# Kernel optimization log

Hardware: AMD Instinct MI355X
Metric: run time of the kernel (lower is better)

Reference implementation:

```python
import jax, jax.numpy as jnp
import numpy as np

HIDDEN = 256
BATCH = 8
N_A = 2048
N_B = 2048


def setup_inputs() -> dict:
    key = jax.random.key(0)
    ks = jax.random.split(key, 9)
    s = 1.0 / np.sqrt(HIDDEN)  # torch Linear default init scale
    return {
        "A": jax.random.normal(ks[0], (BATCH, N_A, HIDDEN), dtype=jnp.float32),
        "B": jax.random.normal(ks[1], (BATCH, N_B, HIDDEN), dtype=jnp.float32),
        "mask_B": jax.random.randint(ks[2], (BATCH, N_B), 0, 2, dtype=jnp.int32),
        "Wq": jax.random.uniform(ks[3], (HIDDEN, HIDDEN), jnp.float32, -s, s),
        "bq": jax.random.uniform(ks[4], (HIDDEN,), jnp.float32, -s, s),
        "Wk": jax.random.uniform(ks[5], (HIDDEN, HIDDEN), jnp.float32, -s, s),
        "bk": jax.random.uniform(ks[6], (HIDDEN,), jnp.float32, -s, s),
        "Wv": jax.random.uniform(ks[7], (HIDDEN, HIDDEN), jnp.float32, -s, s),
        "bv": jax.random.uniform(ks[8], (HIDDEN,), jnp.float32, -s, s),
    }


def reference(A, B, mask_B, Wq, bq, Wk, bk, Wv, bv):
    # QKV projections (torch Linear: x @ W.T + b)
    Q = A @ Wq.T + bq          # [B, N_A, H]
    K = B @ Wk.T + bk          # [B, N_B, H]
    V = B @ Wv.T + bv          # [B, N_B, H]
    scale = 1.0 / jnp.sqrt(jnp.asarray(Q.shape[-1], Q.dtype))
    scores = jnp.einsum("bnh,bmh->bnm", Q, K) * scale  # [B, N_A, N_B]
    neg_inf = jnp.finfo(scores.dtype).min
    scores = jnp.where(mask_B[:, None, :] == 0, neg_inf, scores)
    attn = jax.nn.softmax(scores, axis=-1)
    out = jnp.einsum("bnm,bmh->bnh", attn, V)          # [B, N_A, H]
    return out
```

## Files before the change

### kernel.cpp

```cpp
#include <hip/hip_runtime.h>


typedef __attribute__((ext_vector_type(8))) __bf16 bf16x8;
typedef __attribute__((ext_vector_type(4))) __bf16 bf16x4;
typedef __attribute__((ext_vector_type(4))) float f32x4;

#if __has_builtin(__builtin_amdgcn_exp2f)
#define EXP2(x) __builtin_amdgcn_exp2f(x)
#else
#define EXP2(x) exp2f(x)
#endif

#define MFMA16(a, b, c) __builtin_amdgcn_mfma_f32_16x16x32_bf16((a), (b), (c), 0, 0, 0)

typedef const __attribute__((address_space(1))) char gas_char;
typedef __attribute__((address_space(3))) char las_char;

static __device__ __forceinline__ void gload16(const void* g, void* l) {
  __builtin_amdgcn_global_load_lds((gas_char*)g, (las_char*)l, 16, 0, 0);
}

static __device__ __forceinline__ bf16x8 pack8(f32x4 a, f32x4 b) {
  bf16x8 r;
  r[0] = (__bf16)a[0]; r[1] = (__bf16)a[1]; r[2] = (__bf16)a[2]; r[3] = (__bf16)a[3];
  r[4] = (__bf16)b[0]; r[5] = (__bf16)b[1]; r[6] = (__bf16)b[2]; r[7] = (__bf16)b[3];
  return r;
}

__global__ __launch_bounds__(256) void wprep_kernel(
    const float* __restrict__ Wq, const float* __restrict__ Wk,
    const float* __restrict__ Wv, const int* __restrict__ mask,
    __bf16* __restrict__ Wb, float* __restrict__ mb) {
  const int bid = blockIdx.x;
  if (bid < 96) {
    int c = bid * 256 + threadIdx.x;
    int w_id = c >> 13;
    int j = c & 8191;
    const float* __restrict__ W = (w_id == 0) ? Wq : (w_id == 1 ? Wk : Wv);
    int n = j >> 5;
    int c5 = j & 31;
    int qtr = c5 >> 3;
    int k8 = (c5 & 7) << 3;
    const float* wp = &W[n * 256 + qtr * 64 + k8];
    f32x4 w0 = *(const f32x4*)wp;
    f32x4 w1 = *(const f32x4*)(wp + 4);
    if (w_id == 0) {
      const float cs = 0.090168440f;
      w0[0] *= cs; w0[1] *= cs; w0[2] *= cs; w0[3] *= cs;
      w1[0] *= cs; w1[1] *= cs; w1[2] *= cs; w1[3] *= cs;
    }
    int kx = k8 ^ ((n & 7) << 3);
    *(bf16x8*)&Wb[(size_t)w_id * 65536 + qtr * 16384 + n * 64 + kx] =
        pack8(w0, w1);
  } else {
    int i = (bid - 96) * 256 + threadIdx.x;
    if (i < 8 * 2048) mb[i] = (mask[i] != 0) ? 0.0f : -1.0e30f;
  }
}

__global__ __launch_bounds__(256, 2) void proj_kernel(
    const float* __restrict__ A, const float* __restrict__ Bm,
    const __bf16* __restrict__ Wb,
    const float* __restrict__ bq, const float* __restrict__ bk,
    const float* __restrict__ bv,
    __bf16* __restrict__ QF, __bf16* __restrict__ KF, __bf16* __restrict__ VF) {
  extern __shared__ char smem[];
  const int pid = blockIdx.x;
  const bool isQ = (pid < 256);
  const int rb = (pid & 255) << 6;
  const float* __restrict__ X = isQ ? A : Bm;
  const int tid = threadIdx.x;
  const int w = tid >> 6, l = tid & 63, lo = l & 15, g = l >> 4;
  const int r0 = rb + w * 16;

  bf16x8 xf[8];
#pragma unroll
  for (int q8 = 0; q8 < 8; ++q8) {
    const float* xp = &X[(r0 + lo) * 256 + q8 * 32 + g * 8];
    xf[q8] = pack8(*(const f32x4*)xp, *(const f32x4*)(xp + 4));
  }

  #define STAGEW(srcbase, buf)                                                \
    {                                                                         \
      const char* gw = (srcbase) + w * 1024 + l * 16;                         \
      char* lw = smem + (buf)*32768 + w * 1024;                               \
      gload16(gw, lw);                                                        \
      gload16(gw + 4096, lw + 4096);                                          \
      gload16(gw + 8192, lw + 8192);                                          \
      gload16(gw + 12288, lw + 12288);                                        \
      gload16(gw + 16384, lw + 16384);                                        \
      gload16(gw + 20480, lw + 20480);                                        \
      gload16(gw + 24576, lw + 24576);                                        \
      gload16(gw + 28672, lw + 28672);                                        \
    }

  if (isQ) {
    const char* Wq_ = (const char*)Wb;
    f32x4 acc[16];
#pragma unroll
    for (int j = 0; j < 16; ++j) acc[j] = (f32x4){0.f, 0.f, 0.f, 0.f};

    STAGEW(Wq_, 0);
    __syncthreads();
    for (int qtr = 0; qtr < 4; ++qtr) {
      const int cur = qtr & 1;
      if (qtr < 3) STAGEW(Wq_ + (qtr + 1) * 32768, cur ^ 1);
      const __bf16* Wl = (const __bf16*)(smem + cur * 32768);
#pragma unroll
      for (int ks2 = 0; ks2 < 2; ++ks2) {
        bf16x8 xcur = xf[qtr * 2 + ks2];
#pragma unroll
        for (int nt = 0; nt < 16; ++nt) {
          int n = nt * 16 + lo;
          int kchunk = (ks2 * 4 + g) ^ (n & 7);
          bf16x8 wf = *(const bf16x8*)&Wl[n * 64 + kchunk * 8];
          acc[nt] = MFMA16(xcur, wf, acc[nt]);
        }
      }
      __syncthreads();
    }
    const float cs = 0.090168440f;
    const size_t rgbase = (size_t)(r0 >> 4) << 12;
#pragma unroll
    for (int nt = 0; nt < 16; ++nt) {
      int h = nt * 16 + lo;
      float bb = bq[h] * cs;
      size_t hpart = (size_t)((h >> 5) << 9) + (((h >> 3) & 3) << 7) + (h & 7);
#pragma unroll
      for (int r = 0; r < 4; ++r) {
        int R = r0 + g * 4 + r;
        QF[rgbase + hpart + ((R & 15) << 3)] = (__bf16)(acc[nt][r] + bb);
      }
    }
  } else {
    const char* Wk_ = (const char*)(Wb + 65536);
    const char* Wv_ = (const char*)(Wb + 131072);
    f32x4 accK[16], accV[16];
#pragma unroll
    for (int j = 0; j < 16; ++j) {
      accK[j] = (f32x4){0.f, 0.f, 0.f, 0.f};
      accV[j] = (f32x4){0.f, 0.f, 0.f, 0.f};
    }

    STAGEW(Wk_, 0);
    __syncthreads();
    for (int c = 0; c < 8; ++c) {
      const int cur = c & 1;
      if (c < 7) {
        const int cn = c + 1;
        const char* src = ((cn & 1) ? Wv_ : Wk_) + (cn >> 1) * 32768;
        STAGEW(src, cur ^ 1);
      }
      const __bf16* Wl = (const __bf16*)(smem + cur * 32768);
      const int qtr = c >> 1;
#pragma unroll
      for (int ks2 = 0; ks2 < 2; ++ks2) {
        bf16x8 xcur = xf[qtr * 2 + ks2];
#pragma unroll
        for (int nt = 0; nt < 16; ++nt) {
          int n = nt * 16 + lo;
          int kchunk = (ks2 * 4 + g) ^ (n & 7);
          bf16x8 wf = *(const bf16x8*)&Wl[n * 64 + kchunk * 8];
          if (c & 1) {
            accV[nt] = MFMA16(wf, xcur, accV[nt]);
          } else {
            accK[nt] = MFMA16(xcur, wf, accK[nt]);
          }
        }
      }
      __syncthreads();
    }
    const size_t rgbase = (size_t)(r0 >> 4) << 12;
#pragma unroll
    for (int nt = 0; nt < 16; ++nt) {
      int h = nt * 16 + lo;
      float bb = bk[h];
      size_t hpart = (size_t)((h >> 5) << 9) + (((h >> 3) & 3) << 7) + (h & 7);
#pragma unroll
      for (int r = 0; r < 4; ++r) {
        int R = r0 + g * 4 + r;
        KF[rgbase + hpart + ((R & 15) << 3)] = (__bf16)(accK[nt][r] + bb);
      }
    }
    const int bidx = r0 >> 11;
    const int nb = r0 & 2047;
    __bf16* __restrict__ Vo = VF + (size_t)bidx * 524288;
#pragma unroll
    for (int ht = 0; ht < 16; ++ht)
#pragma unroll
      for (int r = 0; r < 4; ++r) {
        int h = ht * 16 + g * 4 + r;
        int n = nb + lo;
        Vo[((size_t)(n >> 6) << 14) + ((h >> 4) << 10) + (((n >> 3) & 7) << 7) +
           ((h & 15) << 3) + (n & 7)] = (__bf16)(accV[ht][r] + bv[h]);
      }
  }
}

__global__ __launch_bounds__(256, 2) void attn_kernel(
    const __bf16* __restrict__ QF, const __bf16* __restrict__ KF,
    const __bf16* __restrict__ VF, const float* __restrict__ mb,
    __bf16* __restrict__ Opart, float* __restrict__ lpart,
    float* __restrict__ out, int chunk, int direct) {
  extern __shared__ char smem[];
  const int bid = blockIdx.x;
  const int b = bid & 7;
  const int rest = bid >> 3;
  const int qt = rest & 15;
  const int s = rest >> 4;
  const int tid = threadIdx.x;
  const int w = tid >> 6, l = tid & 63, lo = l & 15, g = l >> 4;
  const int q0 = qt * 128 + w * 32;
  const __bf16* __restrict__ Qb = QF + ((size_t)b * 2048 + q0) * 256;
  const __bf16* __restrict__ Kb = KF + (size_t)b * 2048 * 256;
  const __bf16* __restrict__ Vb = VF + (size_t)b * 524288;
  const float* __restrict__ mbb = mb + b * 2048;
  __bf16* Pw = (__bf16*)(smem + 65536) + w * 1280;
  float* mbl = (float*)(smem + 75776);

  bf16x8 qf[2][8];
#pragma unroll
  for (int u = 0; u < 2; ++u)
#pragma unroll
    for (int hs = 0; hs < 8; ++hs)
      qf[u][hs] = *(const bf16x8*)&Qb[u * 4096 + hs * 512 + l * 8];

  f32x4 oacc[2][16];
#pragma unroll
  for (int u = 0; u < 2; ++u)
#pragma unroll
    for (int i = 0; i < 16; ++i) oacc[u][i] = (f32x4){0.f, 0.f, 0.f, 0.f};
  float lsum[2] = {0.f, 0.f};

  const int kv0 = s * chunk;
  const int niter = chunk >> 5;

  #define STAGE_K(kvb, buf)                                                   \
    {                                                                         \
      const char* gk = (const char*)(Kb + (size_t)(kvb) * 256) + w * 4096 +   \
                       l * 16;                                                \
      char* lk = smem + (buf)*16384 + w * 4096;                               \
      gload16(gk, lk);                                                        \
      gload16(gk + 1024, lk + 1024);                                          \
      gload16(gk + 2048, lk + 2048);                                          \
      gload16(gk + 3072, lk + 3072);                                          \
    }
  #define STAGE_V(kvb, buf)                                                   \
    {                                                                         \
      const char* gv = (const char*)(Vb + (((size_t)(kvb) >> 6) << 14) +      \
                                     (((kvb) >> 5) & 1) * 512) +              \
                       w * 8192 + l * 16;                                     \
      char* lv = smem + 32768 + (buf)*16384 + w * 4096;                       \
      gload16(gv, lv);                                                        \
      gload16(gv + 2048, lv + 1024);                                          \
      gload16(gv + 4096, lv + 2048);                                          \
      gload16(gv + 6144, lv + 3072);                                          \
    }

  if (!direct)
    for (int j = tid; j < chunk; j += 256) mbl[j] = mbb[kv0 + j];
  STAGE_K(kv0, 0);
  STAGE_V(kv0, 0);
  __syncthreads();

  for (int it = 0; it < niter; ++it) {
    const int kvb = kv0 + (it << 5);
    const int cur = it & 1;
    const bool pre = (it + 1 < niter);
    if (pre) STAGE_K(kvb + 32, cur ^ 1);
    const char* kbase = smem + cur * 16384;
    const char* vbase = smem + 32768 + cur * 16384;

    f32x4 sacc[2][2];
#pragma unroll
    for (int u = 0; u < 2; ++u)
#pragma unroll
      for (int t = 0; t < 2; ++t) sacc[u][t] = (f32x4){0.f, 0.f, 0.f, 0.f};
    __builtin_amdgcn_s_setprio(1);
#pragma unroll
    for (int t = 0; t < 2; ++t)
#pragma unroll
      for (int hs = 0; hs < 8; ++hs) {
        bf16x8 kf = *(const bf16x8*)(kbase + t * 8192 + hs * 1024 + l * 16);
        sacc[0][t] = MFMA16(kf, qf[0][hs], sacc[0][t]);
        sacc[1][t] = MFMA16(kf, qf[1][hs], sacc[1][t]);
      }
    __builtin_amdgcn_s_setprio(0);

    f32x4 bias4[2];
#pragma unroll
    for (int t = 0; t < 2; ++t) {
      if (direct)
        bias4[t] = *(const f32x4*)&mbb[kvb + t * 16 + g * 4];
      else
        bias4[t] = *(const f32x4*)&mbl[(it << 5) + t * 16 + g * 4];
    }
#pragma unroll
    for (int u = 0; u < 2; ++u)
#pragma unroll
      for (int t = 0; t < 2; ++t) {
        float p0 = EXP2(sacc[u][t][0] + bias4[t][0]);
        float p1 = EXP2(sacc[u][t][1] + bias4[t][1]);
        float p2 = EXP2(sacc[u][t][2] + bias4[t][2]);
        float p3 = EXP2(sacc[u][t][3] + bias4[t][3]);
        lsum[u] += (p0 + p1) + (p2 + p3);
        bf16x4 pk;
        pk[0] = (__bf16)p0; pk[1] = (__bf16)p1;
        pk[2] = (__bf16)p2; pk[3] = (__bf16)p3;
        *(bf16x4*)&Pw[u * 640 + lo * 40 + t * 16 + g * 4] = pk;
      }
    bf16x8 pf[2];
#pragma unroll
    for (int u = 0; u < 2; ++u)
      pf[u] = *(const bf16x8*)&Pw[u * 640 + lo * 40 + g * 8];

    if (direct || !pre) {
      asm volatile("s_waitcnt vmcnt(0)" ::: "memory");
    } else {
      asm volatile("s_waitcnt vmcnt(4)" ::: "memory");
    }
    __builtin_amdgcn_s_barrier();
    __builtin_amdgcn_sched_barrier(0);

    if (pre) STAGE_V(kvb + 32, cur ^ 1);

    __builtin_amdgcn_s_setprio(1);
#pragma unroll
    for (int ht = 0; ht < 16; ++ht) {
      bf16x8 vf = *(const bf16x8*)(vbase + ht * 1024 + l * 16);
      oacc[0][ht] = MFMA16(vf, pf[0], oacc[0][ht]);
      oacc[1][ht] = MFMA16(vf, pf[1], oacc[1][ht]);
    }
    __builtin_amdgcn_s_setprio(0);

    if (direct || !pre) {
      asm volatile("s_waitcnt vmcnt(0)" ::: "memory");
    } else {
      asm volatile("s_waitcnt vmcnt(4)" ::: "memory");
    }
    __builtin_amdgcn_s_barrier();
    __builtin_amdgcn_sched_barrier(0);
  }

#pragma unroll
  for (int u = 0; u < 2; ++u) {
    float ls = lsum[u];
    ls += __shfl_xor(ls, 16);
    ls += __shfl_xor(ls, 32);
    const int q0u = q0 + u * 16;
    if (direct) {
      float inv = 1.0f / ls;
      float* __restrict__ Ob = out + ((size_t)b * 2048 + q0u) * 256;
#pragma unroll
      for (int ht = 0; ht < 16; ++ht) {
        f32x4 v = oacc[u][ht];
        v[0] *= inv; v[1] *= inv; v[2] *= inv; v[3] *= inv;
        *(f32x4*)&Ob[lo * 256 + ht * 16 + g * 4] = v;
      }
    } else {
      const size_t rowbase = (size_t)(s * 8 + b) * 2048 + q0u;
      __bf16* __restrict__ Ob = Opart + rowbase * 256;
#pragma unroll
      for (int ht = 0; ht < 16; ++ht) {
        f32x4 v = oacc[u][ht];
        bf16x4 pk;
        pk[0] = (__bf16)v[0]; pk[1] = (__bf16)v[1];
        pk[2] = (__bf16)v[2]; pk[3] = (__bf16)v[3];
        *(bf16x4*)&Ob[lo * 256 + ht * 16 + g * 4] = pk;
      }
      if (l < 16) lpart[rowbase + lo] = ls;
    }
  }
}

__global__ __launch_bounds__(256) void combine_kernel(
    const __bf16* __restrict__ Opart, const float* __restrict__ lpart,
    float* __restrict__ out, int nsplit) {
  int t = blockIdx.x * 256 + threadIdx.x;
  int row = t >> 6;
  int h4 = (t & 63) << 2;
  f32x4 acc = (f32x4){0.f, 0.f, 0.f, 0.f};
  float denom = 0.f;
  for (int s = 0; s < nsplit; ++s) {
    denom += lpart[s * 16384 + row];
    bf16x4 o = *(const bf16x4*)&Opart[((size_t)s * 16384 + row) * 256 + h4];
    acc[0] += (float)o[0]; acc[1] += (float)o[1];
    acc[2] += (float)o[2]; acc[3] += (float)o[3];
  }
  float inv = 1.0f / denom;
  f32x4 r;
  r[0] = acc[0] * inv; r[1] = acc[1] * inv;
  r[2] = acc[2] * inv; r[3] = acc[3] * inv;
  *(f32x4*)&out[(size_t)row * 256 + h4] = r;
}

extern "C" void kernel_launch(void* const* d_in, const int* in_sizes, int n_in,
                              void* d_out, int out_size, void* d_ws, size_t ws_size,
                              hipStream_t stream) {
  const float* A = (const float*)d_in[0];
  const float* B = (const float*)d_in[1];
  const int* mask = (const int*)d_in[2];
  const float* Wq = (const float*)d_in[3];
  const float* bq = (const float*)d_in[4];
  const float* Wk = (const float*)d_in[5];
  const float* bk = (const float*)d_in[6];
  const float* Wv = (const float*)d_in[7];
  const float* bv = (const float*)d_in[8];

  char* ws = (char*)d_ws;
  __bf16* QF = (__bf16*)(ws);
  __bf16* KF = (__bf16*)(ws + (8ull << 20));
  __bf16* VF = (__bf16*)(ws + (16ull << 20));
  float* mb = (float*)(ws + (24ull << 20));
  float* lpart = (float*)(ws + (24ull << 20) + 0x10000);
  __bf16* Wb = (__bf16*)(ws + (24ull << 20) + 0x90000);
  __bf16* Opart = (__bf16*)(ws + (25ull << 20));

  const size_t base = 25ull << 20;
  const size_t part = 8ull << 20;
  int S;
  if (ws_size >= base + 4 * part) S = 4;
  else if (ws_size >= base + 2 * part) S = 2;
  else if (ws_size >= base + 1 * part) S = 1;
  else S = 0;

  const int PSMEM = 65536;
  (void)hipFuncSetAttribute((const void*)proj_kernel,
                            hipFuncAttributeMaxDynamicSharedMemorySize, PSMEM);
  const int SMEM = 65536 + 4 * 1280 * 2 + 2048;
  (void)hipFuncSetAttribute((const void*)attn_kernel,
                            hipFuncAttributeMaxDynamicSharedMemorySize, SMEM);

  wprep_kernel<<<160, 256, 0, stream>>>(Wq, Wk, Wv, mask, Wb, mb);
  proj_kernel<<<512, 256, PSMEM, stream>>>(A, B, Wb, bq, bk, bv, QF, KF, VF);
  if (S == 0) {
    attn_kernel<<<128, 256, SMEM, stream>>>(QF, KF, VF, mb, nullptr, nullptr,
                                            (float*)d_out, 2048, 1);
  } else {
    attn_kernel<<<128 * S, 256, SMEM, stream>>>(QF, KF, VF, mb, Opart, lpart,
                                                nullptr, 2048 / S, 0);
    combine_kernel<<<4096, 256, 0, stream>>>(Opart, lpart, (float*)d_out, S);
  }
}
```

Measured before the change: 83.27 us.

## Fuse split-K combine into attention via last-block atomic counter; prefetch weights earlier

Removes the separate combine kernel launch. Each attention block increments a per-(batch, query-tile) atomic counter after writing its partial output, and the last arriving block reduces all splits and writes the final output. The counter is zeroed in the weight-prep kernel. The projection kernel also issues the first weight tile's async LDS load before loading and packing the X rows, so the two overlap. The cost is extra fences and atomics, plus a tail of serial combine work done by only the last block of each tile.

```diff
diff --git a/kernel.cpp b/kernel.cpp
--- a/kernel.cpp
+++ b/kernel.cpp
@@ -30,7 +30,7 @@
 __global__ __launch_bounds__(256) void wprep_kernel(
     const float* __restrict__ Wq, const float* __restrict__ Wk,
     const float* __restrict__ Wv, const int* __restrict__ mask,
-    __bf16* __restrict__ Wb, float* __restrict__ mb) {
+    __bf16* __restrict__ Wb, float* __restrict__ mb, int* __restrict__ cnt) {
   const int bid = blockIdx.x;
   if (bid < 96) {
     int c = bid * 256 + threadIdx.x;
@@ -55,6 +55,7 @@
   } else {
     int i = (bid - 96) * 256 + threadIdx.x;
     if (i < 8 * 2048) mb[i] = (mask[i] != 0) ? 0.0f : -1.0e30f;
+    if (i < 128) cnt[i] = 0;
   }
 }
 
@@ -73,13 +74,6 @@
   const int w = tid >> 6, l = tid & 63, lo = l & 15, g = l >> 4;
   const int r0 = rb + w * 16;
 
-  bf16x8 xf[8];
-#pragma unroll
-  for (int q8 = 0; q8 < 8; ++q8) {
-    const float* xp = &X[(r0 + lo) * 256 + q8 * 32 + g * 8];
-    xf[q8] = pack8(*(const f32x4*)xp, *(const f32x4*)(xp + 4));
-  }
-
   #define STAGEW(srcbase, buf)                                                \
     {                                                                         \
       const char* gw = (srcbase) + w * 1024 + l * 16;                         \
@@ -94,14 +88,28 @@
       gload16(gw + 28672, lw + 28672);                                        \
     }
 
+  const char* Wq_ = (const char*)Wb;
+  const char* Wk_ = (const char*)(Wb + 65536);
+  const char* Wv_ = (const char*)(Wb + 131072);
+
   if (isQ) {
-    const char* Wq_ = (const char*)Wb;
+    STAGEW(Wq_, 0);
+  } else {
+    STAGEW(Wk_, 0);
+  }
+
+  bf16x8 xf[8];
+#pragma unroll
+  for (int q8 = 0; q8 < 8; ++q8) {
+    const float* xp = &X[(r0 + lo) * 256 + q8 * 32 + g * 8];
+    xf[q8] = pack8(*(const f32x4*)xp, *(const f32x4*)(xp + 4));
+  }
+  __syncthreads();
+
+  if (isQ) {
     f32x4 acc[16];
 #pragma unroll
     for (int j = 0; j < 16; ++j) acc[j] = (f32x4){0.f, 0.f, 0.f, 0.f};
-
-    STAGEW(Wq_, 0);
-    __syncthreads();
     for (int qtr = 0; qtr < 4; ++qtr) {
       const int cur = qtr & 1;
       if (qtr < 3) STAGEW(Wq_ + (qtr + 1) * 32768, cur ^ 1);
@@ -133,17 +141,12 @@
       }
     }
   } else {
-    const char* Wk_ = (const char*)(Wb + 65536);
-    const char* Wv_ = (const char*)(Wb + 131072);
     f32x4 accK[16], accV[16];
 #pragma unroll
     for (int j = 0; j < 16; ++j) {
       accK[j] = (f32x4){0.f, 0.f, 0.f, 0.f};
       accV[j] = (f32x4){0.f, 0.f, 0.f, 0.f};
     }
-
-    STAGEW(Wk_, 0);
-    __syncthreads();
     for (int c = 0; c < 8; ++c) {
       const int cur = c & 1;
       if (c < 7) {
@@ -201,7 +204,7 @@
     const __bf16* __restrict__ QF, const __bf16* __restrict__ KF,
     const __bf16* __restrict__ VF, const float* __restrict__ mb,
     __bf16* __restrict__ Opart, float* __restrict__ lpart,
-    float* __restrict__ out, int chunk, int direct) {
+    int* __restrict__ cnt, float* __restrict__ out, int chunk, int direct) {
   extern __shared__ char smem[];
   const int bid = blockIdx.x;
   const int b = bid & 7;
@@ -217,6 +220,7 @@
   const float* __restrict__ mbb = mb + b * 2048;
   __bf16* Pw = (__bf16*)(smem + 65536) + w * 1280;
   float* mbl = (float*)(smem + 75776);
+  volatile int* lastflag = (volatile int*)(smem + 77824);
 
   bf16x8 qf[2][8];
 #pragma unroll
@@ -371,27 +375,37 @@
       if (l < 16) lpart[rowbase + lo] = ls;
     }
   }
-}
-
-__global__ __launch_bounds__(256) void combine_kernel(
-    const __bf16* __restrict__ Opart, const float* __restrict__ lpart,
-    float* __restrict__ out, int nsplit) {
-  int t = blockIdx.x * 256 + threadIdx.x;
-  int row = t >> 6;
-  int h4 = (t & 63) << 2;
-  f32x4 acc = (f32x4){0.f, 0.f, 0.f, 0.f};
-  float denom = 0.f;
-  for (int s = 0; s < nsplit; ++s) {
-    denom += lpart[s * 16384 + row];
-    bf16x4 o = *(const bf16x4*)&Opart[((size_t)s * 16384 + row) * 256 + h4];
-    acc[0] += (float)o[0]; acc[1] += (float)o[1];
-    acc[2] += (float)o[2]; acc[3] += (float)o[3];
-  }
-  float inv = 1.0f / denom;
-  f32x4 r;
-  r[0] = acc[0] * inv; r[1] = acc[1] * inv;
-  r[2] = acc[2] * inv; r[3] = acc[3] * inv;
-  *(f32x4*)&out[(size_t)row * 256 + h4] = r;
+
+  if (!direct) {
+    __threadfence();
+    if (tid == 0) {
+      int old = atomicAdd(&cnt[b * 16 + qt], 1);
+      *lastflag = (old == (2048 / chunk) - 1) ? 1 : 0;
+    }
+    __syncthreads();
+    if (*lastflag) {
+      __threadfence();
+      const int nsplit = 2048 / chunk;
+      for (int uu = tid; uu < 128 * 64; uu += 256) {
+        int j = uu >> 6;
+        int h4 = (uu & 63) << 2;
+        f32x4 acc = (f32x4){0.f, 0.f, 0.f, 0.f};
+        float denom = 0.f;
+        for (int s2 = 0; s2 < nsplit; ++s2) {
+          size_t row = (size_t)(s2 * 8 + b) * 2048 + qt * 128 + j;
+          denom += lpart[row];
+          bf16x4 o = *(const bf16x4*)&Opart[row * 256 + h4];
+          acc[0] += (float)o[0]; acc[1] += (float)o[1];
+          acc[2] += (float)o[2]; acc[3] += (float)o[3];
+        }
+        float inv = 1.0f / denom;
+        f32x4 r;
+        r[0] = acc[0] * inv; r[1] = acc[1] * inv;
+        r[2] = acc[2] * inv; r[3] = acc[3] * inv;
+        *(f32x4*)&out[((size_t)b * 2048 + qt * 128 + j) * 256 + h4] = r;
+      }
+    }
+  }
 }
 
 extern "C" void kernel_launch(void* const* d_in, const int* in_sizes, int n_in,
@@ -414,6 +428,7 @@
   float* mb = (float*)(ws + (24ull << 20));
   float* lpart = (float*)(ws + (24ull << 20) + 0x10000);
   __bf16* Wb = (__bf16*)(ws + (24ull << 20) + 0x90000);
+  int* cnt = (int*)(ws + (24ull << 20) + 0xF0000);
   __bf16* Opart = (__bf16*)(ws + (25ull << 20));
 
   const size_t base = 25ull << 20;
@@ -427,18 +442,17 @@
   const int PSMEM = 65536;
   (void)hipFuncSetAttribute((const void*)proj_kernel,
                             hipFuncAttributeMaxDynamicSharedMemorySize, PSMEM);
-  const int SMEM = 65536 + 4 * 1280 * 2 + 2048;
+  const int SMEM = 65536 + 4 * 1280 * 2 + 2048 + 64;
   (void)hipFuncSetAttribute((const void*)attn_kernel,
                             hipFuncAttributeMaxDynamicSharedMemorySize, SMEM);
 
-  wprep_kernel<<<160, 256, 0, stream>>>(Wq, Wk, Wv, mask, Wb, mb);
+  wprep_kernel<<<160, 256, 0, stream>>>(Wq, Wk, Wv, mask, Wb, mb, cnt);
   proj_kernel<<<512, 256, PSMEM, stream>>>(A, B, Wb, bq, bk, bv, QF, KF, VF);
   if (S == 0) {
     attn_kernel<<<128, 256, SMEM, stream>>>(QF, KF, VF, mb, nullptr, nullptr,
-                                            (float*)d_out, 2048, 1);
+                                            cnt, (float*)d_out, 2048, 1);
   } else {
     attn_kernel<<<128 * S, 256, SMEM, stream>>>(QF, KF, VF, mb, Opart, lpart,
-                                                nullptr, 2048 / S, 0);
-    combine_kernel<<<4096, 256, 0, stream>>>(Opart, lpart, (float*)d_out, S);
-  }
-}
+                                                cnt, (float*)d_out, 2048 / S, 0);
+  }
+}
```

Result: slower. 181.4 us (+117.9%).
